# Optimization experiments

Hardware: AMD Instinct MI355X
Metric: run time of the kernel (lower is better)

The kernel has to match this reference:

```python
import jax, jax.numpy as jnp
import numpy as np

B, S, HID = 2, 2048, 2048
N_HEADS, N_KV = 16, 8
HEAD_DIM = HID // N_HEADS  # 128
N_REP = N_HEADS // N_KV


def setup_inputs() -> dict:
    key = jax.random.key(0)
    ks = jax.random.split(key, 5)
    x = jax.random.normal(ks[0], (B, S, HID), dtype=jnp.float32)
    Wq = jax.random.normal(ks[1], (HID, N_HEADS * HEAD_DIM), dtype=jnp.float32) * 0.02
    Wk = jax.random.normal(ks[2], (HID, N_KV * HEAD_DIM), dtype=jnp.float32) * 0.02
    Wv = jax.random.normal(ks[3], (HID, N_KV * HEAD_DIM), dtype=jnp.float32) * 0.02
    Wo = jax.random.normal(ks[4], (N_HEADS * HEAD_DIM, HID), dtype=jnp.float32) * 0.02
    # standard RoPE frequencies: theta_i = 10000^(-2i/head_dim), angle = pos * theta_i
    inv_freq = 1.0 / (10000.0 ** (jnp.arange(0, HEAD_DIM, 2, dtype=jnp.float32) / HEAD_DIM))
    angles = jnp.arange(S, dtype=jnp.float32)[:, None] * inv_freq[None, :]  # [S, HEAD_DIM/2]
    return {
        "x": x, "Wq": Wq, "Wk": Wk, "Wv": Wv, "Wo": Wo,
        "freqs_cos": jnp.cos(angles), "freqs_sin": jnp.sin(angles),
        "start_pos": 0,
    }


def _rope(t, cos, sin):
    # t: [B, S, h, head_dim]; complex-view pairs are (even, odd) along last dim
    tr = t.reshape(*t.shape[:-1], -1, 2)
    re, im = tr[..., 0], tr[..., 1]
    cos = cos[None, :, None, :]
    sin = sin[None, :, None, :]
    out_re = re * cos - im * sin
    out_im = re * sin + im * cos
    return jnp.stack([out_re, out_im], axis=-1).reshape(t.shape)


def reference(x, Wq, Wk, Wv, Wo, freqs_cos, freqs_sin, start_pos):
    b, s, _ = x.shape
    xq = (x @ Wq).reshape(b, s, N_HEADS, HEAD_DIM)
    xk = (x @ Wk).reshape(b, s, N_KV, HEAD_DIM)
    xv = (x @ Wv).reshape(b, s, N_KV, HEAD_DIM)
    xq = _rope(xq, freqs_cos, freqs_sin)
    xk = _rope(xk, freqs_cos, freqs_sin)
    # repeat_kv: each kv head duplicated n_rep times consecutively
    xk = jnp.repeat(xk, N_REP, axis=2)  # [b, s, N_HEADS, hd]
    xv = jnp.repeat(xv, N_REP, axis=2)
    scale = 1.0 / jnp.sqrt(jnp.float32(HEAD_DIM))
    attn = jnp.einsum("bqhd,bkhd->bhqk", xq, xk) * scale
    attn = jax.nn.softmax(attn, axis=-1)
    out = jnp.einsum("bhqk,bkhd->bqhd", attn, xv).reshape(b, s, N_HEADS * HEAD_DIM)
    return out @ Wo
```

## Files before the change

### kernel.cpp

```cpp
#include <hip/hip_runtime.h>
#include <stdint.h>

#define DI __device__ __forceinline__

typedef unsigned short u16;
typedef unsigned int   u32;
typedef __attribute__((ext_vector_type(8))) short short8;
typedef __attribute__((ext_vector_type(4))) float f32x4;


DI u16 f2bf(float f) {
    u32 u = __float_as_uint(f);
    u32 r = u + 0x7fff + ((u >> 16) & 1);
    return (u16)(r >> 16);
}
DI u32 pk2bf(float a, float b) {
    return (u32)f2bf(a) | ((u32)f2bf(b) << 16);
}
DI float bf2f(u16 h) { return __uint_as_float(((u32)h) << 16); }

DI f32x4 mfma16(short8 a, short8 b, f32x4 c) {
    return __builtin_amdgcn_mfma_f32_16x16x32_bf16(a, b, c, 0, 0, 0);
}

DI void gload_lds16(const void* g, void* l) {
    __builtin_amdgcn_global_load_lds(
        (const __attribute__((address_space(1))) void*)g,
        (__attribute__((address_space(3))) void*)l, 16, 0, 0);
}

__global__ __launch_bounds__(256) void cvt_x(const float* __restrict__ x,
                                             u16* __restrict__ o, int n4) {
    int i = blockIdx.x * 256 + threadIdx.x;
    if (i >= n4) return;
    float4 v = *(const float4*)(x + (size_t)i * 4);
    uint2 p; p.x = pk2bf(v.x, v.y); p.y = pk2bf(v.z, v.w);
    *(uint2*)(o + (size_t)i * 4) = p;
}

__global__ __launch_bounds__(256) void transpose_cvt4(const float* __restrict__ W0,
                                                      const float* __restrict__ W1,
                                                      const float* __restrict__ W2,
                                                      const float* __restrict__ W3,
                                                      u16* __restrict__ D0,
                                                      u16* __restrict__ D1,
                                                      u16* __restrict__ D2,
                                                      u16* __restrict__ D3) {
    const float* W; u16* D; int N;
    switch (blockIdx.z) {
        case 0:  W = W0; D = D0; N = 2048; break;
        case 1:  W = W1; D = D1; N = 1024; break;
        case 2:  W = W2; D = D2; N = 1024; break;
        default: W = W3; D = D3; N = 2048; break;
    }
    if ((int)blockIdx.x >= (N >> 6)) return;
    const int K = 2048;
    __shared__ u16 tl[64][65];
    int tx = threadIdx.x & 15, ty = threadIdx.x >> 4;
    int tc = blockIdx.x * 64, tr = blockIdx.y * 64;
#pragma unroll
    for (int i = 0; i < 4; i++) {
        int r = tr + ty + i * 16;
        float4 v = *(const float4*)&W[(size_t)r * N + tc + tx * 4];
        tl[tx*4+0][ty+i*16] = f2bf(v.x);
        tl[tx*4+1][ty+i*16] = f2bf(v.y);
        tl[tx*4+2][ty+i*16] = f2bf(v.z);
        tl[tx*4+3][ty+i*16] = f2bf(v.w);
    }
    __syncthreads();
#pragma unroll
    for (int i = 0; i < 4; i++) {
        int n = tc + ty + i * 16;
        uint2 p;
        p.x = (u32)tl[ty+i*16][tx*4+0] | ((u32)tl[ty+i*16][tx*4+1] << 16);
        p.y = (u32)tl[ty+i*16][tx*4+2] | ((u32)tl[ty+i*16][tx*4+3] << 16);
        *(uint2*)&D[(size_t)n * K + tr + tx * 4] = p;
    }
}

__global__ __launch_bounds__(256) void rope_kernel(u16* __restrict__ buf,
                                                   const float* __restrict__ fc,
                                                   const float* __restrict__ fs,
                                                   int H, int tokshift, int total,
                                                   float oscale) {
    int idx = blockIdx.x * 256 + threadIdx.x;
    if (idx >= total) return;
    int tok = idx >> tokshift;
    int rem = idx & ((1 << tokshift) - 1);
    int h = rem >> 6, j = rem & 63;
    int s = tok & 2047;
    size_t a = ((size_t)tok * H + h) * 128 + 2 * j;
    u32 v = *(u32*)(buf + a);
    float re = bf2f((u16)(v & 0xffff));
    float im = bf2f((u16)(v >> 16));
    float c = fc[s * 64 + j], sn = fs[s * 64 + j];
    *(u32*)(buf + a) = pk2bf((re * c - im * sn) * oscale,
                             (re * sn + im * c) * oscale);
}

__global__ __launch_bounds__(512) void gemm_qkv8(const u16* __restrict__ A,
                                                 const u16* __restrict__ BT,
                                                 u16* __restrict__ Qo,
                                                 u16* __restrict__ Ko,
                                                 u16* __restrict__ Vo) {
    __shared__ __align__(16) u16 SM[65536];
    char* smb = (char*)SM;
    const int tid = threadIdx.x;
    const int w = tid >> 6, l = tid & 63;
    const int l15 = l & 15, lh = l >> 4;
    const int wr = w >> 2, wc = w & 3;

    const int bid = blockIdx.x;
    const int sw = (bid & 7) * 32 + (bid >> 3);
    const int bx = sw & 15, by = sw >> 4;

    const char* Ag = (const char*)A  + (size_t)(by * 256) * 4096;
    const char* Bg = (const char*)BT + (size_t)(bx * 256) * 4096;

    const int r0 = tid >> 3;
    const int c0 = ((tid & 7) << 4) ^ (((tid >> 5) & 1) << 5);
    const int wb = w << 10;

#define STG_A(tt, bb, hh) do {                                              \
        const char* s_ = Ag + (size_t)((hh) * 128 + r0) * 4096 + (tt) * 128 + c0; \
        char* d_ = smb + (bb) * 65536 + (hh) * 16384 + wb;                  \
        gload_lds16(s_, d_);                                                \
        gload_lds16(s_ + (size_t)64 * 4096, d_ + 8192);                     \
    } while (0)
#define STG_B(tt, bb, hh) do {                                              \
        const char* s_ = Bg + (size_t)((hh) * 128 + r0) * 4096 + (tt) * 128 + c0; \
        char* d_ = smb + (bb) * 65536 + 32768 + (hh) * 16384 + wb;          \
        gload_lds16(s_, d_);                                                \
        gload_lds16(s_ + (size_t)64 * 4096, d_ + 8192);                     \
    } while (0)

    const int aoff = l15 * 128 + ((lh * 16) ^ (((l15 >> 2) & 1) << 5));

    const f32x4 fz = {0.f, 0.f, 0.f, 0.f};
    f32x4 acc[8][4];
#pragma unroll
    for (int m = 0; m < 8; m++)
#pragma unroll
        for (int n = 0; n < 4; n++) acc[m][n] = fz;

    STG_A(0, 0, 0); STG_A(0, 0, 1); STG_B(0, 0, 0); STG_B(0, 0, 1);
    STG_A(1, 1, 0);
    asm volatile("s_waitcnt vmcnt(2)" ::: "memory");
    __builtin_amdgcn_s_barrier();

    for (int t = 0; t < 32; ++t) {
        const int cur = t & 1;
        const int t1 = t + 1 < 32 ? t + 1 : 31;
        const int t2 = t + 2 < 32 ? t + 2 : 31;
        const char* Ab = smb + cur * 65536 + wr * 16384 + aoff;
        const char* Bb = smb + cur * 65536 + 32768 + (wc >> 1) * 16384
                         + (wc & 1) * 8192 + aoff;
        short8 aF[4][2], bF[4][2];

        STG_A(t1, cur ^ 1, 1);
#pragma unroll
        for (int m = 0; m < 4; m++) {
            aF[m][0] = *(const short8*)(Ab + m * 2048);
            aF[m][1] = *(const short8*)(Ab + m * 2048 + 64);
        }
#pragma unroll
        for (int n = 0; n < 2; n++) {
            bF[n][0] = *(const short8*)(Bb + n * 2048);
            bF[n][1] = *(const short8*)(Bb + n * 2048 + 64);
        }
        __builtin_amdgcn_s_setprio(1);
#pragma unroll
        for (int m = 0; m < 4; m++)
#pragma unroll
            for (int n = 0; n < 2; n++) {
                acc[m][n] = mfma16(aF[m][0], bF[n][0], acc[m][n]);
                acc[m][n] = mfma16(aF[m][1], bF[n][1], acc[m][n]);
            }
        __builtin_amdgcn_s_setprio(0);
        __builtin_amdgcn_s_barrier();

        STG_B(t1, cur ^ 1, 0);
#pragma unroll
        for (int n = 2; n < 4; n++) {
            bF[n][0] = *(const short8*)(Bb + n * 2048);
            bF[n][1] = *(const short8*)(Bb + n * 2048 + 64);
        }
        __builtin_amdgcn_s_setprio(1);
#pragma unroll
        for (int m = 0; m < 4; m++)
#pragma unroll
            for (int n = 2; n < 4; n++) {
                acc[m][n] = mfma16(aF[m][0], bF[n][0], acc[m][n]);
                acc[m][n] = mfma16(aF[m][1], bF[n][1], acc[m][n]);
            }
        __builtin_amdgcn_s_setprio(0);
        __builtin_amdgcn_s_barrier();

        STG_B(t1, cur ^ 1, 1);
#pragma unroll
        for (int m = 0; m < 4; m++) {
            aF[m][0] = *(const short8*)(Ab + (m + 4) * 2048);
            aF[m][1] = *(const short8*)(Ab + (m + 4) * 2048 + 64);
        }
        __builtin_amdgcn_s_setprio(1);
#pragma unroll
        for (int m = 0; m < 4; m++)
#pragma unroll
            for (int n = 0; n < 2; n++) {
                acc[m + 4][n] = mfma16(aF[m][0], bF[n][0], acc[m + 4][n]);
                acc[m + 4][n] = mfma16(aF[m][1], bF[n][1], acc[m + 4][n]);
            }
        __builtin_amdgcn_s_setprio(0);
        __builtin_amdgcn_s_barrier();

        STG_A(t2, cur, 0);
        __builtin_amdgcn_s_setprio(1);
#pragma unroll
        for (int m = 0; m < 4; m++)
#pragma unroll
            for (int n = 2; n < 4; n++) {
                acc[m + 4][n] = mfma16(aF[m][0], bF[n][0], acc[m + 4][n]);
                acc[m + 4][n] = mfma16(aF[m][1], bF[n][1], acc[m + 4][n]);
            }
        __builtin_amdgcn_s_setprio(0);
        asm volatile("s_waitcnt vmcnt(2)" ::: "memory");
        __builtin_amdgcn_s_barrier();
    }
#undef STG_A
#undef STG_B

    const int rbase = by * 256 + wr * 128 + lh * 4;
    const int cbase = bx * 256 + wc * 64 + l15;
    if (bx < 8) {
#pragma unroll
        for (int m = 0; m < 8; m++)
#pragma unroll
            for (int j = 0; j < 4; j++) {
                size_t ro = (size_t)(rbase + m * 16 + j) * 2048 + cbase;
#pragma unroll
                for (int n = 0; n < 4; n++)
                    Qo[ro + n * 16] = f2bf(acc[m][n][j]);
            }
    } else if (bx < 12) {
        const int ck = cbase - 2048;
#pragma unroll
        for (int m = 0; m < 8; m++)
#pragma unroll
            for (int j = 0; j < 4; j++) {
                size_t ro = (size_t)(rbase + m * 16 + j) * 1024 + ck;
#pragma unroll
                for (int n = 0; n < 4; n++)
                    Ko[ro + n * 16] = f2bf(acc[m][n][j]);
            }
    } else {
#pragma unroll
        for (int m = 0; m < 8; m++)
#pragma unroll
            for (int n = 0; n < 4; n++) {
                int tok = rbase + m * 16;
                int c = cbase + n * 16 - 3072;
                int bb2 = tok >> 11, ss = tok & 2047;
                int h2 = c >> 7, d = c & 127;
                uint2 v;
                v.x = pk2bf(acc[m][n][0], acc[m][n][1]);
                v.y = pk2bf(acc[m][n][2], acc[m][n][3]);
                *(uint2*)(Vo + (size_t)((bb2 * 8 + h2) * 128 + d) * 2048 + ss) = v;
            }
    }
}

__global__ __launch_bounds__(256) void gemm_wo(const u16* __restrict__ A,
                                               const u16* __restrict__ BT,
                                               float* __restrict__ Of,
                                               int M, int N, int K) {
    __shared__ u16 As[128 * 32];
    __shared__ u16 Bs[128 * 32];
    const int tid = threadIdx.x;
    const int w = tid >> 6, l = tid & 63;
    const int m0 = blockIdx.y * 128, n0 = blockIdx.x * 128;
    const int wr = w >> 1, wc = w & 1;
    const int l15 = l & 15, lh = l >> 4;

    const f32x4 fz = {0.f, 0.f, 0.f, 0.f};
    f32x4 acc[4][4];
#pragma unroll
    for (int m = 0; m < 4; m++)
#pragma unroll
        for (int n = 0; n < 4; n++) acc[m][n] = fz;

    const int rowA = w * 32 + (l >> 2);
    const int colb = (l & 3) * 8;

    for (int k0 = 0; k0 < K; k0 += 32) {
        __syncthreads();
#pragma unroll
        for (int c = 0; c < 2; c++) {
            gload_lds16(A  + (size_t)(m0 + rowA + c * 16) * K + k0 + colb,
                        &As[w * 1024 + c * 512]);
            gload_lds16(BT + (size_t)(n0 + rowA + c * 16) * K + k0 + colb,
                        &Bs[w * 1024 + c * 512]);
        }
        __syncthreads();
        short8 af[4], bfr[4];
#pragma unroll
        for (int m = 0; m < 4; m++)
            af[m] = *(const short8*)&As[(wr * 64 + m * 16 + l15) * 32 + lh * 8];
#pragma unroll
        for (int n = 0; n < 4; n++)
            bfr[n] = *(const short8*)&Bs[(wc * 64 + n * 16 + l15) * 32 + lh * 8];
#pragma unroll
        for (int m = 0; m < 4; m++)
#pragma unroll
            for (int n = 0; n < 4; n++)
                acc[m][n] = mfma16(af[m], bfr[n], acc[m][n]);
    }

    const int rbase = m0 + wr * 64 + lh * 4;
    const int cbase = n0 + wc * 64 + l15;
#pragma unroll
    for (int m = 0; m < 4; m++)
#pragma unroll
        for (int j = 0; j < 4; j++) {
            size_t ro = (size_t)(rbase + m * 16 + j) * N + cbase;
#pragma unroll
            for (int n = 0; n < 4; n++)
                Of[ro + n * 16] = acc[m][n][j];
        }
}

__global__ __launch_bounds__(256, 2) void attn_kernel(const u16* __restrict__ Q,
                                                      const u16* __restrict__ Kg,
                                                      const u16* __restrict__ Vg,
                                                      u16* __restrict__ O) {
    __shared__ __align__(16) u16 Ks[2][8192];
    __shared__ __align__(16) u16 Vs[2][8192];
    __shared__ __align__(16) u16 Ps[4][2048];
    const int tid = threadIdx.x;
    const int w = tid >> 6, l = tid & 63;
    const int qt = blockIdx.x, bh = blockIdx.y;
    const int b = bh >> 4, h = bh & 15, h2 = h >> 1;
    const int l15 = l & 15, lh = l >> 4;

    char* KsB = (char*)&Ks[0][0];
    char* VsB = (char*)&Vs[0][0];
    char* PsB = (char*)&Ps[w][0];

    const char* Kbase = (const char*)Kg + (size_t)b * 2048 * 2048 + h2 * 256;
    const char* Vbase = (const char*)Vg + (size_t)(b * 8 + h2) * 128 * 4096;
    int krow[4], kcol[4], vrow[4], vcol[4];
#pragma unroll
    for (int c = 0; c < 4; c++) {
        int X = c * 4096 + tid * 16;
        krow[c] = X >> 8; kcol[c] = (X & 255) ^ ((krow[c] & 7) << 4);
        vrow[c] = X >> 7; vcol[c] = (X & 127) ^ ((vrow[c] & 7) << 4);
    }

#define STAGE(t, pb) do {                                               \
        const char* Kt = Kbase + (size_t)(t) * 131072;                  \
        const char* Vt = Vbase + (t) * 128;                             \
        char* kd = KsB + (pb) * 16384 + tid * 16;                       \
        char* vd = VsB + (pb) * 16384 + tid * 16;                       \
        _Pragma("unroll")                                               \
        for (int c = 0; c < 4; c++) {                                   \
            gload_lds16(Kt + krow[c] * 2048 + kcol[c], kd + c * 4096);  \
            gload_lds16(Vt + (size_t)vrow[c] * 4096 + vcol[c], vd + c * 4096); \
        }                                                               \
    } while (0)

    short8 qf0[4], qf1[4];
    {
        const u16* qp = Q + ((size_t)(b * 2048 + qt * 128 + w * 32 + l15)) * 2048
                          + h * 128 + lh * 8;
#pragma unroll
        for (int ks = 0; ks < 4; ks++) {
            qf0[ks] = *(const short8*)(qp + ks * 32);
            qf1[ks] = *(const short8*)(qp + 16 * 2048 + ks * 32);
        }
    }

    const f32x4 fz = {0.f, 0.f, 0.f, 0.f};
    f32x4 o0[8], o1[8];
#pragma unroll
    for (int n = 0; n < 8; n++) { o0[n] = fz; o1[n] = fz; }
    float mrow0[4] = {-1e30f, -1e30f, -1e30f, -1e30f};
    float mrow1[4] = {-1e30f, -1e30f, -1e30f, -1e30f};
    float lsum0[4] = {0.f, 0.f, 0.f, 0.f};
    float lsum1[4] = {0.f, 0.f, 0.f, 0.f};

    STAGE(0, 0);

    for (int t = 0; t < 32; t++) {
        __syncthreads();
        const int pb = t & 1;
        if (t < 31) STAGE(t + 1, pb ^ 1);
        const char* kc = KsB + pb * 16384;
        const char* vc = VsB + pb * 16384;
        const int swz = (l15 & 7) << 4;

        f32x4 s0[4], s1[4];
#pragma unroll
        for (int ct = 0; ct < 4; ct++) {
            s0[ct] = fz; s1[ct] = fz;
#pragma unroll
            for (int ks = 0; ks < 4; ks++) {
                short8 kf = *(const short8*)(kc + ((ct * 16 + l15) << 8)
                                                + ((ks * 64 + lh * 16) ^ swz));
                s0[ct] = mfma16(qf0[ks], kf, s0[ct]);
                s1[ct] = mfma16(qf1[ks], kf, s1[ct]);
            }
        }

        float pl0[4], pl1[4];
#pragma unroll
        for (int r = 0; r < 4; r++) {
            pl0[r] = fmaxf(fmaxf(s0[0][r], s0[1][r]), fmaxf(s0[2][r], s0[3][r]));
            pl1[r] = fmaxf(fmaxf(s1[0][r], s1[1][r]), fmaxf(s1[2][r], s1[3][r]));
        }
        bool grow = false;
#pragma unroll
        for (int r = 0; r < 4; r++)
            grow = grow || (pl0[r] > mrow0[r] + 8.f) || (pl1[r] > mrow1[r] + 8.f);
        if (__any(grow)) {
#pragma unroll
            for (int r = 0; r < 4; r++) {
                float mx = pl0[r];
                mx = fmaxf(mx, __shfl_xor(mx, 1));
                mx = fmaxf(mx, __shfl_xor(mx, 2));
                mx = fmaxf(mx, __shfl_xor(mx, 4));
                mx = fmaxf(mx, __shfl_xor(mx, 8));
                float mnew = fmaxf(mrow0[r], mx);
                float fsc = exp2f(mrow0[r] - mnew);
                mrow0[r] = mnew;
                lsum0[r] *= fsc;
#pragma unroll
                for (int n = 0; n < 8; n++) o0[n][r] *= fsc;
            }
#pragma unroll
            for (int r = 0; r < 4; r++) {
                float mx = pl1[r];
                mx = fmaxf(mx, __shfl_xor(mx, 1));
                mx = fmaxf(mx, __shfl_xor(mx, 2));
                mx = fmaxf(mx, __shfl_xor(mx, 4));
                mx = fmaxf(mx, __shfl_xor(mx, 8));
                float mnew = fmaxf(mrow1[r], mx);
                float fsc = exp2f(mrow1[r] - mnew);
                mrow1[r] = mnew;
                lsum1[r] *= fsc;
#pragma unroll
                for (int n = 0; n < 8; n++) o1[n][r] *= fsc;
            }
        }
        const int cb2 = l15 << 1;
#pragma unroll
        for (int r = 0; r < 4; r++) {
            float p0 = exp2f(s0[0][r] - mrow0[r]);
            float p1 = exp2f(s0[1][r] - mrow0[r]);
            float p2 = exp2f(s0[2][r] - mrow0[r]);
            float p3 = exp2f(s0[3][r] - mrow0[r]);
            lsum0[r] += (p0 + p1) + (p2 + p3);
            const int rw = lh * 4 + r;
            const int rb = rw << 7;
            const int sw2 = (rw & 7) << 4;
            *(u16*)(PsB + (rb + (( 0 + cb2) ^ sw2))) =
                (u16)((__float_as_uint(p0) + 0x8000u) >> 16);
            *(u16*)(PsB + (rb + ((32 + cb2) ^ sw2))) =
                (u16)((__float_as_uint(p1) + 0x8000u) >> 16);
            *(u16*)(PsB + (rb + ((64 + cb2) ^ sw2))) =
                (u16)((__float_as_uint(p2) + 0x8000u) >> 16);
            *(u16*)(PsB + (rb + ((96 + cb2) ^ sw2))) =
                (u16)((__float_as_uint(p3) + 0x8000u) >> 16);
        }
#pragma unroll
        for (int r = 0; r < 4; r++) {
            float p0 = exp2f(s1[0][r] - mrow1[r]);
            float p1 = exp2f(s1[1][r] - mrow1[r]);
            float p2 = exp2f(s1[2][r] - mrow1[r]);
            float p3 = exp2f(s1[3][r] - mrow1[r]);
            lsum1[r] += (p0 + p1) + (p2 + p3);
            const int rw = 16 + lh * 4 + r;
            const int rb = rw << 7;
            const int sw2 = (rw & 7) << 4;
            *(u16*)(PsB + (rb + (( 0 + cb2) ^ sw2))) =
                (u16)((__float_as_uint(p0) + 0x8000u) >> 16);
            *(u16*)(PsB + (rb + ((32 + cb2) ^ sw2))) =
                (u16)((__float_as_uint(p1) + 0x8000u) >> 16);
            *(u16*)(PsB + (rb + ((64 + cb2) ^ sw2))) =
                (u16)((__float_as_uint(p2) + 0x8000u) >> 16);
            *(u16*)(PsB + (rb + ((96 + cb2) ^ sw2))) =
                (u16)((__float_as_uint(p3) + 0x8000u) >> 16);
        }

#pragma unroll
        for (int ks2 = 0; ks2 < 2; ks2++) {
            short8 pf0 = *(const short8*)(PsB + ((l15 << 7)
                                + ((ks2 * 64 + lh * 16) ^ swz)));
            short8 pf1 = *(const short8*)(PsB + (((16 + l15) << 7)
                                + ((ks2 * 64 + lh * 16) ^ swz)));
#pragma unroll
            for (int n = 0; n < 8; n++) {
                short8 vf = *(const short8*)(vc + (((n * 16 + l15) << 7)
                                                  + ((ks2 * 64 + lh * 16) ^ swz)));
                o0[n] = mfma16(pf0, vf, o0[n]);
                o1[n] = mfma16(pf1, vf, o1[n]);
            }
        }
    }

    const size_t ob0 = ((size_t)(b * 2048 + qt * 128 + w * 32 + lh * 4)) * 2048
                       + h * 128 + l15;
#pragma unroll
    for (int r = 0; r < 4; r++) {
        float ls = lsum0[r];
        ls += __shfl_xor(ls, 1);
        ls += __shfl_xor(ls, 2);
        ls += __shfl_xor(ls, 4);
        ls += __shfl_xor(ls, 8);
        float li = 1.0f / ls;
#pragma unroll
        for (int n = 0; n < 8; n++)
            O[ob0 + (size_t)r * 2048 + n * 16] = f2bf(o0[n][r] * li);
    }
    const size_t ob1 = ob0 + (size_t)16 * 2048;
#pragma unroll
    for (int r = 0; r < 4; r++) {
        float ls = lsum1[r];
        ls += __shfl_xor(ls, 1);
        ls += __shfl_xor(ls, 2);
        ls += __shfl_xor(ls, 4);
        ls += __shfl_xor(ls, 8);
        float li = 1.0f / ls;
#pragma unroll
        for (int n = 0; n < 8; n++)
            O[ob1 + (size_t)r * 2048 + n * 16] = f2bf(o1[n][r] * li);
    }
#undef STAGE
}

extern "C" void kernel_launch(void* const* d_in, const int* in_sizes, int n_in,
                              void* d_out, int out_size, void* d_ws, size_t ws_size,
                              hipStream_t stream) {
    const float* x  = (const float*)d_in[0];
    const float* Wq = (const float*)d_in[1];
    const float* Wk = (const float*)d_in[2];
    const float* Wv = (const float*)d_in[3];
    const float* Wo = (const float*)d_in[4];
    const float* fc = (const float*)d_in[5];
    const float* fs = (const float*)d_in[6];
    float* out = (float*)d_out;

    uint8_t* ws = (uint8_t*)d_ws;
    u16* xb   = (u16*)(ws + 0);
    u16* wqkv = (u16*)(ws + 16777216);
    u16* wqT  = (u16*)(ws + 16777216);
    u16* wkT  = (u16*)(ws + 25165824);
    u16* wvT  = (u16*)(ws + 29360128);
    u16* woT  = (u16*)(ws + 33554432);
    u16* qb   = (u16*)(ws + 41943040);
    u16* kb   = (u16*)(ws + 58720256);
    u16* vT   = (u16*)(ws + 67108864);
    u16* ao   = xb;

    cvt_x<<<dim3(8192), dim3(256), 0, stream>>>(x, xb, 2097152);
    transpose_cvt4<<<dim3(32, 32, 4), dim3(256), 0, stream>>>(Wq, Wk, Wv, Wo,
                                                              wqT, wkT, wvT, woT);

    gemm_qkv8<<<dim3(256), dim3(512), 0, stream>>>(xb, wqkv, qb, kb, vT);

    rope_kernel<<<dim3(16384), dim3(256), 0, stream>>>(qb, fc, fs, 16, 10, 4194304,
                                                       0.12751742987f);
    rope_kernel<<<dim3(8192),  dim3(256), 0, stream>>>(kb, fc, fs, 8, 9, 2097152, 1.0f);

    attn_kernel<<<dim3(16, 32), dim3(256), 0, stream>>>(qb, kb, vT, ao);

    gemm_wo<<<dim3(16, 32), dim3(256), 0, stream>>>(ao, woT, out, 4096, 2048, 2048);
}
```

Baseline: 256.0 us.

## Split attention KV range in two, fuse Q RoPE, add combine kernel

The attention kernel now splits the key/value sequence into two halves per query tile (flash-decoding style). Each half writes an unnormalized output plus per-row max and sum, and a new combine kernel merges the two halves. This doubles the grid to 1024 blocks and halves the LDS tiles so four blocks fit per CU, aiming for better occupancy and fewer waves. RoPE and the softmax scale for Q are now applied inside the attention kernel when Q fragments are loaded, which removes the separate Q rope pass. The cost is an extra combine kernel, extra bf16 output traffic, and a bf16 rounding of the unnormalized partial outputs.

```diff
diff --git a/kernel.cpp b/kernel.cpp
--- a/kernel.cpp
+++ b/kernel.cpp
@@ -27,6 +27,22 @@
     __builtin_amdgcn_global_load_lds(
         (const __attribute__((address_space(1))) void*)g,
         (__attribute__((address_space(3))) void*)l, 16, 0, 0);
+}
+
+DI short8 rope8(short8 raw, const float* cp, const float* sp, float osc) {
+    float4 c4 = *(const float4*)cp;
+    float4 s4 = *(const float4*)sp;
+    u32* rp = (u32*)&raw;
+#pragma unroll
+    for (int p = 0; p < 4; p++) {
+        u32 v = rp[p];
+        float re = __uint_as_float(v << 16);
+        float im = __uint_as_float(v & 0xffff0000u);
+        float cc = ((const float*)&c4)[p] * osc;
+        float ss = ((const float*)&s4)[p] * osc;
+        rp[p] = pk2bf(re * cc - im * ss, re * ss + im * cc);
+    }
+    return raw;
 }
 
 __global__ __launch_bounds__(256) void cvt_x(const float* __restrict__ x,
@@ -328,16 +344,23 @@
         }
 }
 
-__global__ __launch_bounds__(256, 2) void attn_kernel(const u16* __restrict__ Q,
+__global__ __launch_bounds__(256, 4) void attn_kernel(const u16* __restrict__ Q,
                                                       const u16* __restrict__ Kg,
                                                       const u16* __restrict__ Vg,
-                                                      u16* __restrict__ O) {
-    __shared__ __align__(16) u16 Ks[2][8192];
-    __shared__ __align__(16) u16 Vs[2][8192];
-    __shared__ __align__(16) u16 Ps[4][2048];
+                                                      const float* __restrict__ fc,
+                                                      const float* __restrict__ fs,
+                                                      u16* __restrict__ O0,
+                                                      u16* __restrict__ O1,
+                                                      float2* __restrict__ ML) {
+    __shared__ __align__(16) u16 Ks[2][4096];
+    __shared__ __align__(16) u16 Vs[2][4096];
+    __shared__ __align__(16) u16 Ps[4][1024];
     const int tid = threadIdx.x;
     const int w = tid >> 6, l = tid & 63;
-    const int qt = blockIdx.x, bh = blockIdx.y;
+    const int bid = blockIdx.x;
+    const int y = (bid & 7) | ((bid >> 7) << 3);
+    const int qt = (bid >> 3) & 15;
+    const int bh = y >> 1, half = y & 1;
     const int b = bh >> 4, h = bh & 15, h2 = h >> 1;
     const int l15 = l & 15, lh = l >> 4;
 
@@ -345,36 +368,44 @@
     char* VsB = (char*)&Vs[0][0];
     char* PsB = (char*)&Ps[w][0];
 
-    const char* Kbase = (const char*)Kg + (size_t)b * 2048 * 2048 + h2 * 256;
-    const char* Vbase = (const char*)Vg + (size_t)(b * 8 + h2) * 128 * 4096;
-    int krow[4], kcol[4], vrow[4], vcol[4];
-#pragma unroll
-    for (int c = 0; c < 4; c++) {
-        int X = c * 4096 + tid * 16;
-        krow[c] = X >> 8; kcol[c] = (X & 255) ^ ((krow[c] & 7) << 4);
-        vrow[c] = X >> 7; vcol[c] = (X & 127) ^ ((vrow[c] & 7) << 4);
-    }
+    const char* Kbase = (const char*)Kg + (size_t)b * 2048 * 2048 + h2 * 256
+                        + (size_t)half * 1024 * 2048;
+    const char* Vbase = (const char*)Vg + (size_t)(b * 8 + h2) * 128 * 4096
+                        + half * 2048;
+    const int X0 = tid * 16, X1 = 4096 + tid * 16;
+    const int kr0 = X0 >> 8, kc0 = (X0 & 255) ^ ((kr0 & 7) << 4);
+    const int kr1 = X1 >> 8, kc1 = (X1 & 255) ^ ((kr1 & 7) << 4);
+    const int vr0 = X0 >> 6,
+              vc0 = (X0 & 63) ^ ((vr0 & 3) << 4) ^ (((vr0 >> 2) & 1) << 5);
+    const int vr1 = X1 >> 6,
+              vc1 = (X1 & 63) ^ ((vr1 & 3) << 4) ^ (((vr1 >> 2) & 1) << 5);
 
 #define STAGE(t, pb) do {                                               \
-        const char* Kt = Kbase + (size_t)(t) * 131072;                  \
-        const char* Vt = Vbase + (t) * 128;                             \
-        char* kd = KsB + (pb) * 16384 + tid * 16;                       \
-        char* vd = VsB + (pb) * 16384 + tid * 16;                       \
-        _Pragma("unroll")                                               \
-        for (int c = 0; c < 4; c++) {                                   \
-            gload_lds16(Kt + krow[c] * 2048 + kcol[c], kd + c * 4096);  \
-            gload_lds16(Vt + (size_t)vrow[c] * 4096 + vcol[c], vd + c * 4096); \
-        }                                                               \
+        const char* Kt = Kbase + (size_t)(t) * 65536;                   \
+        const char* Vt = Vbase + (t) * 64;                              \
+        char* kd = KsB + (pb) * 8192 + tid * 16;                        \
+        char* vd = VsB + (pb) * 8192 + tid * 16;                        \
+        gload_lds16(Kt + kr0 * 2048 + kc0, kd);                         \
+        gload_lds16(Kt + kr1 * 2048 + kc1, kd + 4096);                  \
+        gload_lds16(Vt + (size_t)vr0 * 4096 + vc0, vd);                 \
+        gload_lds16(Vt + (size_t)vr1 * 4096 + vc1, vd + 4096);          \
     } while (0)
 
+    const float OSC = 0.12751742987f;
     short8 qf0[4], qf1[4];
     {
-        const u16* qp = Q + ((size_t)(b * 2048 + qt * 128 + w * 32 + l15)) * 2048
-                          + h * 128 + lh * 8;
+        const int s0r = qt * 128 + w * 32 + l15;
+        const int s1r = s0r + 16;
+        const u16* qp0 = Q + ((size_t)(b * 2048 + s0r)) * 2048 + h * 128 + lh * 8;
+        const u16* qp1 = Q + ((size_t)(b * 2048 + s1r)) * 2048 + h * 128 + lh * 8;
 #pragma unroll
         for (int ks = 0; ks < 4; ks++) {
-            qf0[ks] = *(const short8*)(qp + ks * 32);
-            qf1[ks] = *(const short8*)(qp + 16 * 2048 + ks * 32);
+            qf0[ks] = rope8(*(const short8*)(qp0 + ks * 32),
+                            &fc[s0r * 64 + ks * 16 + lh * 4],
+                            &fs[s0r * 64 + ks * 16 + lh * 4], OSC);
+            qf1[ks] = rope8(*(const short8*)(qp1 + ks * 32),
+                            &fc[s1r * 64 + ks * 16 + lh * 4],
+                            &fs[s1r * 64 + ks * 16 + lh * 4], OSC);
         }
     }
 
@@ -387,24 +418,26 @@
     float lsum0[4] = {0.f, 0.f, 0.f, 0.f};
     float lsum1[4] = {0.f, 0.f, 0.f, 0.f};
 
+    const int kswz = (l15 & 7) << 4;
+    const int vswz = ((l15 & 3) << 4) ^ (((l15 >> 2) & 1) << 5);
+
     STAGE(0, 0);
 
     for (int t = 0; t < 32; t++) {
         __syncthreads();
         const int pb = t & 1;
         if (t < 31) STAGE(t + 1, pb ^ 1);
-        const char* kc = KsB + pb * 16384;
-        const char* vc = VsB + pb * 16384;
-        const int swz = (l15 & 7) << 4;
-
-        f32x4 s0[4], s1[4];
-#pragma unroll
-        for (int ct = 0; ct < 4; ct++) {
+        const char* kcp = KsB + pb * 8192;
+        const char* vcp = VsB + pb * 8192;
+
+        f32x4 s0[2], s1[2];
+#pragma unroll
+        for (int ct = 0; ct < 2; ct++) {
             s0[ct] = fz; s1[ct] = fz;
 #pragma unroll
             for (int ks = 0; ks < 4; ks++) {
-                short8 kf = *(const short8*)(kc + ((ct * 16 + l15) << 8)
-                                                + ((ks * 64 + lh * 16) ^ swz));
+                short8 kf = *(const short8*)(kcp + (ct * 16 + l15) * 256
+                                                 + ((ks * 64 + lh * 16) ^ kswz));
                 s0[ct] = mfma16(qf0[ks], kf, s0[ct]);
                 s1[ct] = mfma16(qf1[ks], kf, s1[ct]);
             }
@@ -413,8 +446,8 @@
         float pl0[4], pl1[4];
 #pragma unroll
         for (int r = 0; r < 4; r++) {
-            pl0[r] = fmaxf(fmaxf(s0[0][r], s0[1][r]), fmaxf(s0[2][r], s0[3][r]));
-            pl1[r] = fmaxf(fmaxf(s1[0][r], s1[1][r]), fmaxf(s1[2][r], s1[3][r]));
+            pl0[r] = fmaxf(s0[0][r], s0[1][r]);
+            pl1[r] = fmaxf(s1[0][r], s1[1][r]);
         }
         bool grow = false;
 #pragma unroll
@@ -450,64 +483,47 @@
                 for (int n = 0; n < 8; n++) o1[n][r] *= fsc;
             }
         }
-        const int cb2 = l15 << 1;
+        const int cb2 = l15 * 2;
 #pragma unroll
         for (int r = 0; r < 4; r++) {
             float p0 = exp2f(s0[0][r] - mrow0[r]);
             float p1 = exp2f(s0[1][r] - mrow0[r]);
-            float p2 = exp2f(s0[2][r] - mrow0[r]);
-            float p3 = exp2f(s0[3][r] - mrow0[r]);
-            lsum0[r] += (p0 + p1) + (p2 + p3);
+            lsum0[r] += p0 + p1;
             const int rw = lh * 4 + r;
-            const int rb = rw << 7;
-            const int sw2 = (rw & 7) << 4;
-            *(u16*)(PsB + (rb + (( 0 + cb2) ^ sw2))) =
+            const int sw2 = (r << 4) ^ ((lh & 1) << 5);
+            *(u16*)(PsB + rw * 64 + (cb2 ^ sw2)) =
                 (u16)((__float_as_uint(p0) + 0x8000u) >> 16);
-            *(u16*)(PsB + (rb + ((32 + cb2) ^ sw2))) =
+            *(u16*)(PsB + rw * 64 + ((32 + cb2) ^ sw2)) =
                 (u16)((__float_as_uint(p1) + 0x8000u) >> 16);
-            *(u16*)(PsB + (rb + ((64 + cb2) ^ sw2))) =
-                (u16)((__float_as_uint(p2) + 0x8000u) >> 16);
-            *(u16*)(PsB + (rb + ((96 + cb2) ^ sw2))) =
-                (u16)((__float_as_uint(p3) + 0x8000u) >> 16);
         }
 #pragma unroll
         for (int r = 0; r < 4; r++) {
             float p0 = exp2f(s1[0][r] - mrow1[r]);
             float p1 = exp2f(s1[1][r] - mrow1[r]);
-            float p2 = exp2f(s1[2][r] - mrow1[r]);
-            float p3 = exp2f(s1[3][r] - mrow1[r]);
-            lsum1[r] += (p0 + p1) + (p2 + p3);
+            lsum1[r] += p0 + p1;
             const int rw = 16 + lh * 4 + r;
-            const int rb = rw << 7;
-            const int sw2 = (rw & 7) << 4;
-            *(u16*)(PsB + (rb + (( 0 + cb2) ^ sw2))) =
+            const int sw2 = (r << 4) ^ ((lh & 1) << 5);
+            *(u16*)(PsB + rw * 64 + (cb2 ^ sw2)) =
                 (u16)((__float_as_uint(p0) + 0x8000u) >> 16);
-            *(u16*)(PsB + (rb + ((32 + cb2) ^ sw2))) =
+            *(u16*)(PsB + rw * 64 + ((32 + cb2) ^ sw2)) =
                 (u16)((__float_as_uint(p1) + 0x8000u) >> 16);
-            *(u16*)(PsB + (rb + ((64 + cb2) ^ sw2))) =
-                (u16)((__float_as_uint(p2) + 0x8000u) >> 16);
-            *(u16*)(PsB + (rb + ((96 + cb2) ^ sw2))) =
-                (u16)((__float_as_uint(p3) + 0x8000u) >> 16);
-        }
-
-#pragma unroll
-        for (int ks2 = 0; ks2 < 2; ks2++) {
-            short8 pf0 = *(const short8*)(PsB + ((l15 << 7)
-                                + ((ks2 * 64 + lh * 16) ^ swz)));
-            short8 pf1 = *(const short8*)(PsB + (((16 + l15) << 7)
-                                + ((ks2 * 64 + lh * 16) ^ swz)));
-#pragma unroll
-            for (int n = 0; n < 8; n++) {
-                short8 vf = *(const short8*)(vc + (((n * 16 + l15) << 7)
-                                                  + ((ks2 * 64 + lh * 16) ^ swz)));
-                o0[n] = mfma16(pf0, vf, o0[n]);
-                o1[n] = mfma16(pf1, vf, o1[n]);
-            }
-        }
-    }
-
-    const size_t ob0 = ((size_t)(b * 2048 + qt * 128 + w * 32 + lh * 4)) * 2048
-                       + h * 128 + l15;
+        }
+
+        short8 pf0 = *(const short8*)(PsB + l15 * 64 + ((lh * 16) ^ vswz));
+        short8 pf1 = *(const short8*)(PsB + (16 + l15) * 64 + ((lh * 16) ^ vswz));
+#pragma unroll
+        for (int n = 0; n < 8; n++) {
+            short8 vf = *(const short8*)(vcp + (n * 16 + l15) * 64
+                                             + ((lh * 16) ^ vswz));
+            o0[n] = mfma16(pf0, vf, o0[n]);
+            o1[n] = mfma16(pf1, vf, o1[n]);
+        }
+    }
+
+    u16* Op = half ? O1 : O0;
+    const int q0 = qt * 128 + w * 32;
+    const size_t ob0 = ((size_t)(b * 2048 + q0 + lh * 4)) * 2048 + h * 128 + l15;
+    const int mlb = half * 65536 + (b * 16 + h) * 2048 + q0;
 #pragma unroll
     for (int r = 0; r < 4; r++) {
         float ls = lsum0[r];
@@ -515,10 +531,10 @@
         ls += __shfl_xor(ls, 2);
         ls += __shfl_xor(ls, 4);
         ls += __shfl_xor(ls, 8);
-        float li = 1.0f / ls;
+        if (l15 == 0) ML[mlb + lh * 4 + r] = make_float2(mrow0[r], ls);
 #pragma unroll
         for (int n = 0; n < 8; n++)
-            O[ob0 + (size_t)r * 2048 + n * 16] = f2bf(o0[n][r] * li);
+            Op[ob0 + (size_t)r * 2048 + n * 16] = f2bf(o0[n][r]);
     }
     const size_t ob1 = ob0 + (size_t)16 * 2048;
 #pragma unroll
@@ -528,12 +544,42 @@
         ls += __shfl_xor(ls, 2);
         ls += __shfl_xor(ls, 4);
         ls += __shfl_xor(ls, 8);
-        float li = 1.0f / ls;
+        if (l15 == 0) ML[mlb + 16 + lh * 4 + r] = make_float2(mrow1[r], ls);
 #pragma unroll
         for (int n = 0; n < 8; n++)
-            O[ob1 + (size_t)r * 2048 + n * 16] = f2bf(o1[n][r] * li);
+            Op[ob1 + (size_t)r * 2048 + n * 16] = f2bf(o1[n][r]);
     }
 #undef STAGE
+}
+
+__global__ __launch_bounds__(256) void attn_combine(const u16* __restrict__ A,
+                                                    const u16* __restrict__ Bv,
+                                                    const float2* __restrict__ ML,
+                                                    u16* __restrict__ O) {
+    int idx = blockIdx.x * 256 + threadIdx.x;
+    size_t e = (size_t)idx * 8;
+    int hh = (int)((e >> 7) & 15);
+    int s  = (int)((e >> 11) & 2047);
+    int b  = (int)(e >> 22);
+    int mi = (b * 16 + hh) * 2048 + s;
+    float2 a0 = ML[mi], a1 = ML[65536 + mi];
+    float M = fmaxf(a0.x, a1.x);
+    float e0 = exp2f(a0.x - M), e1 = exp2f(a1.x - M);
+    float inv = 1.0f / (a0.y * e0 + a1.y * e1);
+    e0 *= inv; e1 *= inv;
+    short8 v0 = *(const short8*)(A + e);
+    short8 v1 = *(const short8*)(Bv + e);
+    uint4 ov;
+    u32* op = (u32*)&ov;
+#pragma unroll
+    for (int j = 0; j < 4; j++) {
+        u32 w0 = ((u32*)&v0)[j], w1 = ((u32*)&v1)[j];
+        float lo = __uint_as_float(w0 << 16) * e0 + __uint_as_float(w1 << 16) * e1;
+        float hi = __uint_as_float(w0 & 0xffff0000u) * e0
+                 + __uint_as_float(w1 & 0xffff0000u) * e1;
+        op[j] = pk2bf(lo, hi);
+    }
+    *(uint4*)(O + e) = ov;
 }
 
 extern "C" void kernel_launch(void* const* d_in, const int* in_sizes, int n_in,
@@ -558,7 +604,9 @@
     u16* qb   = (u16*)(ws + 41943040);
     u16* kb   = (u16*)(ws + 58720256);
     u16* vT   = (u16*)(ws + 67108864);
-    u16* ao   = xb;
+    float2* ml = (float2*)(ws + 75497472);
+    u16* o0   = xb;
+    u16* o1   = wqkv;
 
     cvt_x<<<dim3(8192), dim3(256), 0, stream>>>(x, xb, 2097152);
     transpose_cvt4<<<dim3(32, 32, 4), dim3(256), 0, stream>>>(Wq, Wk, Wv, Wo,
@@ -566,11 +614,11 @@
 
     gemm_qkv8<<<dim3(256), dim3(512), 0, stream>>>(xb, wqkv, qb, kb, vT);
 
-    rope_kernel<<<dim3(16384), dim3(256), 0, stream>>>(qb, fc, fs, 16, 10, 4194304,
-                                                       0.12751742987f);
-    rope_kernel<<<dim3(8192),  dim3(256), 0, stream>>>(kb, fc, fs, 8, 9, 2097152, 1.0f);
-
-    attn_kernel<<<dim3(16, 32), dim3(256), 0, stream>>>(qb, kb, vT, ao);
-
-    gemm_wo<<<dim3(16, 32), dim3(256), 0, stream>>>(ao, woT, out, 4096, 2048, 2048);
-}
+    rope_kernel<<<dim3(8192), dim3(256), 0, stream>>>(kb, fc, fs, 8, 9, 2097152, 1.0f);
+
+    attn_kernel<<<dim3(1024), dim3(256), 0, stream>>>(qb, kb, vT, fc, fs,
+                                                      o0, o1, ml);
+    attn_combine<<<dim3(4096), dim3(256), 0, stream>>>(o0, o1, ml, o0);
+
+    gemm_wo<<<dim3(16, 32), dim3(256), 0, stream>>>(o0, woT, out, 4096, 2048, 2048);
+}
```

After: 605.5 us. 2.37x slower.
